# Optimization experiments

Measured on AMD Instinct MI355X. Metric: run time of the kernel, lower is better.

Reference implementation:

```python
import jax, jax.numpy as jnp
import numpy as np

D_MODEL = 512
N_HEADS = 8
D_FF = 2048
B, L = 4, 2048
EPS = 1e-5


def _layernorm(x, g, b):
    mu = jnp.mean(x, axis=-1, keepdims=True)
    var = jnp.mean(jnp.square(x - mu), axis=-1, keepdims=True)
    return (x - mu) * jax.lax.rsqrt(var + EPS) * g + b


def setup_inputs() -> dict:
    key = jax.random.key(0)
    ks = jax.random.split(key, 8)
    s = 0.02
    return {
        'x': jax.random.normal(ks[0], (B, L, D_MODEL), jnp.float32),
        'Wq': jax.random.normal(ks[1], (D_MODEL, D_MODEL), jnp.float32) * s,
        'bq': jnp.zeros((D_MODEL,), jnp.float32),
        'Wk': jax.random.normal(ks[2], (D_MODEL, D_MODEL), jnp.float32) * s,
        'bk': jnp.zeros((D_MODEL,), jnp.float32),
        'Wv': jax.random.normal(ks[3], (D_MODEL, D_MODEL), jnp.float32) * s,
        'bv': jnp.zeros((D_MODEL,), jnp.float32),
        'Wo': jax.random.normal(ks[4], (D_MODEL, D_MODEL), jnp.float32) * s,
        'bo': jnp.zeros((D_MODEL,), jnp.float32),
        'W1': jax.random.normal(ks[5], (D_MODEL, D_FF), jnp.float32) * s,
        'b1': jnp.zeros((D_FF,), jnp.float32),
        'W2': jax.random.normal(ks[6], (D_FF, D_MODEL), jnp.float32) * s,
        'b2': jnp.zeros((D_MODEL,), jnp.float32),
        'g1': jnp.ones((D_MODEL,), jnp.float32),
        'be1': jnp.zeros((D_MODEL,), jnp.float32),
        'g2': jnp.ones((D_MODEL,), jnp.float32),
        'be2': jnp.zeros((D_MODEL,), jnp.float32),
    }


def reference(x, Wq, bq, Wk, bk, Wv, bv, Wo, bo, W1, b1, W2, b2, g1, be1, g2, be2):
    B_, L_, D = x.shape
    H = N_HEADS
    E = D // H
    q = (x @ Wq + bq).reshape(B_, L_, H, E)
    k = (x @ Wk + bk).reshape(B_, L_, H, E)
    v = (x @ Wv + bv).reshape(B_, L_, H, E)
    scale = 1.0 / jnp.sqrt(jnp.float32(E))
    # full [B,H,L,S] scores (mask_flag=False -> no causal mask)
    scores = jnp.einsum('blhe,bshe->bhls', q, k)
    A = jax.nn.softmax(scale * scores, axis=-1)
    V = jnp.einsum('bhls,bshd->blhd', A, v).reshape(B_, L_, D)
    attn_out = V @ Wo + bo
    x = _layernorm(x + attn_out, g1, be1)
    h = jax.nn.gelu(x @ W1 + b1, approximate=False)  # torch nn.GELU default = exact erf
    x = _layernorm(x + (h @ W2 + b2), g2, be2)
    return x
```

## Files before the change

kernel.cpp:

```cpp
#include <hip/hip_runtime.h>
#include <math.h>

#define DM 512
#define LSEQ 2048
#define BATCH 4
#define NH 8
#define EH 64
#define DFF 2048
#define MTOK (BATCH*LSEQ)
#define QKVW 1536
#define QSCL 0.18033688011112042f

using short8  = __attribute__((ext_vector_type(8))) short;
using floatx4 = __attribute__((ext_vector_type(4))) float;

__device__ __forceinline__ short f2b(float f) {
    unsigned u = __float_as_uint(f);
    return (short)((u + 0x7FFFu + ((u >> 16) & 1u)) >> 16);
}
__device__ __forceinline__ float b2f(short s) {
    return __uint_as_float(((unsigned)(unsigned short)s) << 16);
}
__device__ __forceinline__ unsigned pack2bf(float lo, float hi) {
    return __builtin_amdgcn_perm(__float_as_uint(hi) + 0x8000u,
                                 __float_as_uint(lo) + 0x8000u, 0x07060302u);
}
__device__ __forceinline__ float gelu_tanh(float v) {
    float v2 = v * v;
    float y  = v * fmaf(0.0356774081f, v2, 0.7978845608f);
    float e  = __builtin_amdgcn_exp2f(y * 2.885390082f);
    float r  = __builtin_amdgcn_rcpf(e + 1.0f);
    return v * (1.0f - r);
}
__device__ __forceinline__ void load_lds16(const short* g, short* l) {
    __builtin_amdgcn_global_load_lds(
        (const __attribute__((address_space(1))) void*)g,
        (__attribute__((address_space(3))) void*)l, 16, 0, 0);
}
#define MFMA_BF16(a, b, c) __builtin_amdgcn_mfma_f32_16x16x32_bf16(a, b, c, 0, 0, 0)

__global__ __launch_bounds__(256) void prep_kernel(
    const float* __restrict__ Wq, const float* __restrict__ Wk,
    const float* __restrict__ Wv, const float* __restrict__ Wo,
    const float* __restrict__ W1, const float* __restrict__ W2,
    const float* __restrict__ x,
    const float* __restrict__ bq, const float* __restrict__ bk,
    const float* __restrict__ bv,
    short* __restrict__ Wqkvt, short* __restrict__ Wot,
    short* __restrict__ W1t, short* __restrict__ W2t,
    short* __restrict__ xb, float* __restrict__ bqkv)
{
    __shared__ float t[64][65];
    const int bid = blockIdx.x;
    const int tid = threadIdx.x;

    if (bid >= 2880) {
        #pragma unroll
        for (int j = 0; j < 6; ++j) {
            const int i = j * 256 + tid;
            bqkv[i] = (i < 512) ? bq[i] : (i < 1024 ? bk[i - 512] : bv[i - 1024]);
        }
        return;
    }
    if (bid >= 832) {
        const long i = ((long)(bid - 832) * 256 + tid) * 8;
        float4 a = *(const float4*)(x + i);
        float4 b = *(const float4*)(x + i + 4);
        short tt[8] = { f2b(a.x), f2b(a.y), f2b(a.z), f2b(a.w),
                        f2b(b.x), f2b(b.y), f2b(b.z), f2b(b.w) };
        *(float4*)(xb + i) = *(float4*)tt;
        return;
    }
    const float* src; short* dst; int C, R, bx, by;
    if (bid < 256) {
        const int w = bid >> 6, sub = bid & 63;
        src = (w == 0) ? Wq : (w == 1) ? Wk : Wv;
        dst = Wqkvt + (long)w * 262144;
        R = 512; C = 512; bx = sub & 7; by = sub >> 3;
    } else if (bid < 320) {
        const int sub = bid - 256;
        src = Wo; dst = Wot; R = 512; C = 512; bx = sub & 7; by = sub >> 3;
    } else if (bid < 576) {
        const int sub = bid - 320;
        src = W1; dst = W1t; R = 512; C = 2048; bx = sub & 31; by = sub >> 5;
    } else {
        const int sub = bid - 576;
        src = W2; dst = W2t; R = 2048; C = 512; bx = sub & 7; by = sub >> 3;
    }
    const int r0 = by * 64, c0 = bx * 64;
    const int r = tid >> 2, cs = (tid & 3) * 16;
    const float* ip = src + (long)(r0 + r) * C + c0 + cs;
    #pragma unroll
    for (int i = 0; i < 4; ++i) {
        float4 v = *(const float4*)(ip + i * 4);
        t[r][cs + i*4 + 0] = v.x; t[r][cs + i*4 + 1] = v.y;
        t[r][cs + i*4 + 2] = v.z; t[r][cs + i*4 + 3] = v.w;
    }
    __syncthreads();
    short tmp[16];
    #pragma unroll
    for (int j = 0; j < 16; ++j) tmp[j] = f2b(t[cs + j][r]);
    short* op = dst + (long)(c0 + r) * R + r0 + cs;
    *(float4*)op       = *(float4*)&tmp[0];
    *(float4*)(op + 8) = *(float4*)&tmp[8];
}

template<int TN, int DO_GELU, int QKV>
__global__ __launch_bounds__(256, 4) void mfma_gemm(
    const short* __restrict__ A, const short* __restrict__ Bt,
    const float* __restrict__ bias, short* __restrict__ C,
    short* __restrict__ VtOut, int M, int N, int K, int lda, int ldc)
{
    constexpr int NJ = TN / 32;
    constexpr int NB = TN / 64;
    __shared__ short As[2][128][32];
    __shared__ short Bs[2][TN][32];

    const int tid  = threadIdx.x;
    const int wave = tid >> 6;
    const int lane = tid & 63;
    const int qd   = lane >> 4;
    const int sl   = lane & 15;
    const int m0 = blockIdx.y * 128;
    const int n0 = blockIdx.x * TN;
    const int wm = (wave & 1) * 64;
    const int wn = (wave >> 1) * (TN / 2);
    const int srow = lane >> 2;
    const int scol = (lane & 3) * 8;

    floatx4 acc[4][NJ];
    const floatx4 fz = {0.f, 0.f, 0.f, 0.f};
    #pragma unroll
    for (int i = 0; i < 4; ++i)
        #pragma unroll
        for (int j = 0; j < NJ; ++j) acc[i][j] = fz;

    const short* Abase = A  + (long)m0 * lda + scol;
    const short* Bbase = Bt + (long)n0 * K   + scol;

    #pragma unroll
    for (int it = 0; it < 2; ++it) {
        const int rg = wave * 2 + it;
        load_lds16(Abase + (long)(rg*16 + srow) * lda, &As[0][rg * 16][0]);
    }
    #pragma unroll
    for (int it = 0; it < NB; ++it) {
        const int rg = wave * NB + it;
        load_lds16(Bbase + (long)(rg*16 + srow) * K, &Bs[0][rg * 16][0]);
    }

    const int NIT = K / 32;
    for (int kit = 0; kit < NIT; ++kit) {
        const int cur = kit & 1;
        __syncthreads();
        if (kit + 1 < NIT) {
            const int nk = (kit + 1) * 32;
            #pragma unroll
            for (int it = 0; it < 2; ++it) {
                const int rg = wave * 2 + it;
                load_lds16(Abase + (long)(rg*16 + srow) * lda + nk, &As[1 - cur][rg * 16][0]);
            }
            #pragma unroll
            for (int it = 0; it < NB; ++it) {
                const int rg = wave * NB + it;
                load_lds16(Bbase + (long)(rg*16 + srow) * K + nk, &Bs[1 - cur][rg * 16][0]);
            }
        }
        short8 af[4], bf[NJ];
        #pragma unroll
        for (int t = 0; t < 4; ++t)
            af[t] = *(const short8*)&As[cur][wm + t*16 + sl][qd * 8];
        #pragma unroll
        for (int t = 0; t < NJ; ++t)
            bf[t] = *(const short8*)&Bs[cur][wn + t*16 + sl][qd * 8];
        #pragma unroll
        for (int i = 0; i < 4; ++i)
            #pragma unroll
            for (int j = 0; j < NJ; ++j)
                acc[i][j] = MFMA_BF16(af[i], bf[j], acc[i][j]);
    }

    #pragma unroll
    for (int j = 0; j < NJ; ++j) {
        const int col = n0 + wn + j*16 + sl;
        const float bvs = bias[col];
        #pragma unroll
        for (int i = 0; i < 4; ++i) {
            float v[4];
            #pragma unroll
            for (int r = 0; r < 4; ++r) {
                float tv = acc[i][j][r] + bvs;
                if (DO_GELU) tv = gelu_tanh(tv);
                v[r] = tv;
            }
            const int row0 = m0 + wm + i*16 + qd*4;
            if (QKV) {
                if (col < 1024) {
                    const float s = (col < 512) ? QSCL : 1.0f;
                    #pragma unroll
                    for (int r = 0; r < 4; ++r)
                        C[(long)(row0 + r) * 1024 + col] = f2b(v[r] * s);
                } else {
                    const int e = col - 1024;
                    const int b_ = row0 >> 11, l0 = row0 & 2047;
                    uint2 w;
                    w.x = pack2bf(v[0], v[1]);
                    w.y = pack2bf(v[2], v[3]);
                    *(uint2*)&VtOut[(((long)(b_*8 + (e >> 6))) * 64 + (e & 63)) * 2048 + l0] = w;
                }
            } else {
                #pragma unroll
                for (int r = 0; r < 4; ++r)
                    C[(long)(row0 + r) * ldc + col] = f2b(v[r]);
            }
        }
    }
}

__global__ __launch_bounds__(256, 3) void mfma_attn(
    const short* __restrict__ QK, const short* __restrict__ VtG,
    short* __restrict__ O)
{
    __shared__ short Ks[2][2][64][32];
    __shared__ short Vs[2][2][64][32];
    __shared__ short PT[4][16][72];

    const int tid  = threadIdx.x;
    const int wave = tid >> 6;
    const int lane = tid & 63;
    const int qd   = lane >> 4;
    const int sl   = lane & 15;
    const int srow = lane >> 2;
    const int scol = (lane & 3) * 8;

    const int bid = blockIdx.x;
    const int h  = bid & 7;
    const int b  = (bid >> 3) & 3;
    const int qt = bid >> 5;
    const int tok0 = b * LSEQ;
    const int q0 = qt * 64;

    const short* Kbase = QK + (long)tok0 * 1024 + 512 + h * EH
                         + (long)(wave*16 + srow) * 1024 + scol;
    const short* Vbase = VtG + ((long)(b * NH + h)) * EH * 2048
                         + (long)(wave*16 + srow) * 2048 + scol;

    {
        const int qr = lane >> 2;
        const int qc = (lane & 3) * 16;
        const short* qp = QK + (long)(tok0 + q0 + wave*16 + qr) * 1024 + h * EH + qc;
        short* dp = &PT[wave][qr][qc];
        *(float4*)dp       = *(const float4*)qp;
        *(float4*)(dp + 8) = *(const float4*)(qp + 8);
    }
    short8 aq[2];
    #pragma unroll
    for (int ks = 0; ks < 2; ++ks)
        aq[ks] = *(const short8*)&PT[wave][sl][ks*32 + qd*8];

    float l_i = 0.f;
    floatx4 oacc[4];
    const floatx4 fz = {0.f, 0.f, 0.f, 0.f};
    #pragma unroll
    for (int t = 0; t < 4; ++t) oacc[t] = fz;

    #pragma unroll
    for (int p = 0; p < 2; ++p) {
        load_lds16(Kbase + p*32, &Ks[0][p][wave*16][0]);
        load_lds16(Vbase + p*32, &Vs[0][p][wave*16][0]);
    }

    for (int kt = 0; kt < 32; ++kt) {
        const int cur = kt & 1;
        __syncthreads();
        if (kt + 1 < 32) {
            #pragma unroll
            for (int p = 0; p < 2; ++p) {
                load_lds16(Kbase + (long)(kt+1)*64*1024 + p*32, &Ks[1 - cur][p][wave*16][0]);
                load_lds16(Vbase + (kt+1)*64 + p*32,            &Vs[1 - cur][p][wave*16][0]);
            }
        }

        floatx4 sT[4];
        #pragma unroll
        for (int t = 0; t < 4; ++t) sT[t] = fz;
        #pragma unroll
        for (int ks = 0; ks < 2; ++ks)
            #pragma unroll
            for (int t = 0; t < 4; ++t) {
                short8 ak = *(const short8*)&Ks[cur][ks][t*16 + sl][qd * 8];
                sT[t] = MFMA_BF16(ak, aq[ks], sT[t]);
            }

        #pragma unroll
        for (int t = 0; t < 4; ++t) {
            const float p0 = __builtin_amdgcn_exp2f(sT[t][0]);
            const float p1 = __builtin_amdgcn_exp2f(sT[t][1]);
            const float p2 = __builtin_amdgcn_exp2f(sT[t][2]);
            const float p3 = __builtin_amdgcn_exp2f(sT[t][3]);
            l_i += (p0 + p1) + (p2 + p3);
            uint2 w;
            w.x = pack2bf(p0, p1);
            w.y = pack2bf(p2, p3);
            *(uint2*)&PT[wave][sl][t*16 + qd*4] = w;
        }

        #pragma unroll
        for (int ks = 0; ks < 2; ++ks) {
            short8 ap = *(const short8*)&PT[wave][sl][ks*32 + qd*8];
            #pragma unroll
            for (int t = 0; t < 4; ++t) {
                short8 bv = *(const short8*)&Vs[cur][ks][t*16 + sl][qd * 8];
                oacc[t] = MFMA_BF16(ap, bv, oacc[t]);
            }
        }
    }

    l_i += __shfl_xor(l_i, 16);
    l_i += __shfl_xor(l_i, 32);
    float linv[4];
    #pragma unroll
    for (int r = 0; r < 4; ++r)
        linv[r] = 1.0f / __shfl(l_i, qd*4 + r, 64);

    #pragma unroll
    for (int t = 0; t < 4; ++t)
        #pragma unroll
        for (int r = 0; r < 4; ++r) {
            const int row = tok0 + q0 + wave*16 + qd*4 + r;
            const int col = h * EH + t*16 + sl;
            O[(long)row * DM + col] = f2b(oacc[t][r] * linv[r]);
        }
}

template<int X_BF16, int OUT_F32>
__global__ __launch_bounds__(256) void add_ln_kernel(
    const void* __restrict__ Xv, const short* __restrict__ R,
    const float* __restrict__ g, const float* __restrict__ beta,
    void* __restrict__ outv)
{
    const int row = blockIdx.x;
    const int tid = threadIdx.x;
    float x0, x1;
    if (X_BF16) {
        const short* xp = (const short*)Xv + (long)row * DM;
        x0 = b2f(xp[tid]); x1 = b2f(xp[tid + 256]);
    } else {
        const float* xp = (const float*)Xv + (long)row * DM;
        x0 = xp[tid]; x1 = xp[tid + 256];
    }
    const short* rp = R + (long)row * DM;
    const float v0 = x0 + b2f(rp[tid]);
    const float v1 = x1 + b2f(rp[tid + 256]);
    float s = v0 + v1, sq = v0*v0 + v1*v1;
    #pragma unroll
    for (int o = 32; o > 0; o >>= 1) {
        s  += __shfl_down(s, o);
        sq += __shfl_down(sq, o);
    }
    __shared__ float ss[4], ssq[4];
    const int wid = tid >> 6, lane = tid & 63;
    if (lane == 0) { ss[wid] = s; ssq[wid] = sq; }
    __syncthreads();
    const float S  = ss[0] + ss[1] + ss[2] + ss[3];
    const float SQ = ssq[0] + ssq[1] + ssq[2] + ssq[3];
    const float mean = S * (1.0f / DM);
    const float var  = SQ * (1.0f / DM) - mean * mean;
    const float rstd = rsqrtf(var + 1e-5f);
    const float o0 = (v0 - mean) * rstd * g[tid] + beta[tid];
    const float o1 = (v1 - mean) * rstd * g[tid + 256] + beta[tid + 256];
    if (OUT_F32) {
        float* op = (float*)outv + (long)row * DM;
        op[tid] = o0; op[tid + 256] = o1;
    } else {
        short* op = (short*)outv + (long)row * DM;
        op[tid] = f2b(o0); op[tid + 256] = f2b(o1);
    }
}

extern "C" void kernel_launch(void* const* d_in, const int* in_sizes, int n_in,
                              void* d_out, int out_size, void* d_ws, size_t ws_size,
                              hipStream_t stream)
{
    const float* x   = (const float*)d_in[0];
    const float* Wq  = (const float*)d_in[1];
    const float* bq  = (const float*)d_in[2];
    const float* Wk  = (const float*)d_in[3];
    const float* bk  = (const float*)d_in[4];
    const float* Wv  = (const float*)d_in[5];
    const float* bv  = (const float*)d_in[6];
    const float* Wo  = (const float*)d_in[7];
    const float* bo  = (const float*)d_in[8];
    const float* W1  = (const float*)d_in[9];
    const float* b1  = (const float*)d_in[10];
    const float* W2  = (const float*)d_in[11];
    const float* b2  = (const float*)d_in[12];
    const float* g1  = (const float*)d_in[13];
    const float* be1 = (const float*)d_in[14];
    const float* g2  = (const float*)d_in[15];
    const float* be2 = (const float*)d_in[16];
    float* out = (float*)d_out;

    short* ws    = (short*)d_ws;
    short* Wqkvt = ws;
    short* Wot   = Wqkvt + 786432;
    short* W1t   = Wot + 262144;
    short* W2t   = W1t + 1048576;
    float* bqkv  = (float*)(W2t + 1048576);
    short* xb    = (short*)(bqkv + 1536);
    short* qk    = xb + 4194304;
    short* VtG   = qk + 8388608;
    short* Ob    = VtG + 4194304;
    short* res   = Ob + 4194304;
    short* hbuf  = qk;

    const dim3 blk(256);

    prep_kernel<<<dim3(2881), blk, 0, stream>>>(
        Wq, Wk, Wv, Wo, W1, W2, x, bq, bk, bv,
        Wqkvt, Wot, W1t, W2t, xb, bqkv);

    mfma_gemm<128, 0, 1><<<dim3(12, 64), blk, 0, stream>>>(
        xb, Wqkvt, bqkv, qk, VtG, MTOK, QKVW, DM, DM, 0);

    mfma_attn<<<dim3(1024), blk, 0, stream>>>(qk, VtG, Ob);

    mfma_gemm<64, 0, 0><<<dim3(8, 64), blk, 0, stream>>>(
        Ob, Wot, bo, res, nullptr, MTOK, DM, DM, DM, DM);

    add_ln_kernel<0, 0><<<dim3(MTOK), blk, 0, stream>>>(x, res, g1, be1, xb);

    mfma_gemm<128, 1, 0><<<dim3(16, 64), blk, 0, stream>>>(
        xb, W1t, b1, hbuf, nullptr, MTOK, DFF, DM, DM, DFF);

    mfma_gemm<64, 0, 0><<<dim3(8, 64), blk, 0, stream>>>(
        hbuf, W2t, b2, res, nullptr, MTOK, DM, DFF, DFF, DM);

    add_ln_kernel<1, 1><<<dim3(MTOK), blk, 0, stream>>>(xb, res, g2, be2, out);
}
```

Measured before the change: 291.3 us.

## Process 32 query rows per wave in attention to reuse K/V tiles

Each wave in the attention kernel now handles two 16-row query sub-tiles instead of one, doubling the block's query tile to 128 rows and halving the grid to 512 blocks. Each K and V fragment read from LDS feeds two MFMAs, which halves K/V global and LDS traffic per query. The cost is more registers per thread (accumulators and scores are doubled), so the occupancy hint drops from 3 to 2 blocks per CU, and there are fewer blocks to spread across the CUs.

New measurement: 276.7 us. 1.05x faster.

```diff
diff --git a/kernel.cpp b/kernel.cpp
--- a/kernel.cpp
+++ b/kernel.cpp
@@ -217,13 +217,13 @@
     }
 }
 
-__global__ __launch_bounds__(256, 3) void mfma_attn(
+__global__ __launch_bounds__(256, 2) void mfma_attn(
     const short* __restrict__ QK, const short* __restrict__ VtG,
     short* __restrict__ O)
 {
     __shared__ short Ks[2][2][64][32];
     __shared__ short Vs[2][2][64][32];
-    __shared__ short PT[4][16][72];
+    __shared__ short PT[4][32][72];
 
     const int tid  = threadIdx.x;
     const int wave = tid >> 6;
@@ -238,7 +238,7 @@
     const int b  = (bid >> 3) & 3;
     const int qt = bid >> 5;
     const int tok0 = b * LSEQ;
-    const int q0 = qt * 64;
+    const int q0 = qt * 128;
 
     const short* Kbase = QK + (long)tok0 * 1024 + 512 + h * EH
                          + (long)(wave*16 + srow) * 1024 + scol;
@@ -246,23 +246,29 @@
                          + (long)(wave*16 + srow) * 2048 + scol;
 
     {
-        const int qr = lane >> 2;
-        const int qc = (lane & 3) * 16;
-        const short* qp = QK + (long)(tok0 + q0 + wave*16 + qr) * 1024 + h * EH + qc;
+        const int qr = lane >> 1;
+        const int qc = (lane & 1) * 32;
+        const short* qp = QK + (long)(tok0 + q0 + wave*32 + qr) * 1024 + h * EH + qc;
         short* dp = &PT[wave][qr][qc];
-        *(float4*)dp       = *(const float4*)qp;
-        *(float4*)(dp + 8) = *(const float4*)(qp + 8);
-    }
-    short8 aq[2];
-    #pragma unroll
-    for (int ks = 0; ks < 2; ++ks)
-        aq[ks] = *(const short8*)&PT[wave][sl][ks*32 + qd*8];
-
-    float l_i = 0.f;
-    floatx4 oacc[4];
+        *(float4*)dp        = *(const float4*)qp;
+        *(float4*)(dp + 8)  = *(const float4*)(qp + 8);
+        *(float4*)(dp + 16) = *(const float4*)(qp + 16);
+        *(float4*)(dp + 24) = *(const float4*)(qp + 24);
+    }
+    short8 aq[2][2];
+    #pragma unroll
+    for (int q2 = 0; q2 < 2; ++q2)
+        #pragma unroll
+        for (int ks = 0; ks < 2; ++ks)
+            aq[q2][ks] = *(const short8*)&PT[wave][q2*16 + sl][ks*32 + qd*8];
+
+    float l_i[2] = {0.f, 0.f};
+    floatx4 oacc[2][4];
     const floatx4 fz = {0.f, 0.f, 0.f, 0.f};
     #pragma unroll
-    for (int t = 0; t < 4; ++t) oacc[t] = fz;
+    for (int q2 = 0; q2 < 2; ++q2)
+        #pragma unroll
+        for (int t = 0; t < 4; ++t) oacc[q2][t] = fz;
 
     #pragma unroll
     for (int p = 0; p < 2; ++p) {
@@ -281,56 +287,69 @@
             }
         }
 
-        floatx4 sT[4];
-        #pragma unroll
-        for (int t = 0; t < 4; ++t) sT[t] = fz;
+        floatx4 sT[2][4];
+        #pragma unroll
+        for (int q2 = 0; q2 < 2; ++q2)
+            #pragma unroll
+            for (int t = 0; t < 4; ++t) sT[q2][t] = fz;
         #pragma unroll
         for (int ks = 0; ks < 2; ++ks)
             #pragma unroll
             for (int t = 0; t < 4; ++t) {
                 short8 ak = *(const short8*)&Ks[cur][ks][t*16 + sl][qd * 8];
-                sT[t] = MFMA_BF16(ak, aq[ks], sT[t]);
-            }
-
-        #pragma unroll
-        for (int t = 0; t < 4; ++t) {
-            const float p0 = __builtin_amdgcn_exp2f(sT[t][0]);
-            const float p1 = __builtin_amdgcn_exp2f(sT[t][1]);
-            const float p2 = __builtin_amdgcn_exp2f(sT[t][2]);
-            const float p3 = __builtin_amdgcn_exp2f(sT[t][3]);
-            l_i += (p0 + p1) + (p2 + p3);
-            uint2 w;
-            w.x = pack2bf(p0, p1);
-            w.y = pack2bf(p2, p3);
-            *(uint2*)&PT[wave][sl][t*16 + qd*4] = w;
-        }
+                sT[0][t] = MFMA_BF16(ak, aq[0][ks], sT[0][t]);
+                sT[1][t] = MFMA_BF16(ak, aq[1][ks], sT[1][t]);
+            }
+
+        #pragma unroll
+        for (int q2 = 0; q2 < 2; ++q2)
+            #pragma unroll
+            for (int t = 0; t < 4; ++t) {
+                const float p0 = __builtin_amdgcn_exp2f(sT[q2][t][0]);
+                const float p1 = __builtin_amdgcn_exp2f(sT[q2][t][1]);
+                const float p2 = __builtin_amdgcn_exp2f(sT[q2][t][2]);
+                const float p3 = __builtin_amdgcn_exp2f(sT[q2][t][3]);
+                l_i[q2] += (p0 + p1) + (p2 + p3);
+                uint2 w;
+                w.x = pack2bf(p0, p1);
+                w.y = pack2bf(p2, p3);
+                *(uint2*)&PT[wave][q2*16 + sl][t*16 + qd*4] = w;
+            }
 
         #pragma unroll
         for (int ks = 0; ks < 2; ++ks) {
-            short8 ap = *(const short8*)&PT[wave][sl][ks*32 + qd*8];
+            short8 ap0 = *(const short8*)&PT[wave][sl][ks*32 + qd*8];
+            short8 ap1 = *(const short8*)&PT[wave][16 + sl][ks*32 + qd*8];
             #pragma unroll
             for (int t = 0; t < 4; ++t) {
                 short8 bv = *(const short8*)&Vs[cur][ks][t*16 + sl][qd * 8];
-                oacc[t] = MFMA_BF16(ap, bv, oacc[t]);
+                oacc[0][t] = MFMA_BF16(ap0, bv, oacc[0][t]);
+                oacc[1][t] = MFMA_BF16(ap1, bv, oacc[1][t]);
             }
         }
     }
 
-    l_i += __shfl_xor(l_i, 16);
-    l_i += __shfl_xor(l_i, 32);
-    float linv[4];
-    #pragma unroll
-    for (int r = 0; r < 4; ++r)
-        linv[r] = 1.0f / __shfl(l_i, qd*4 + r, 64);
-
-    #pragma unroll
-    for (int t = 0; t < 4; ++t)
-        #pragma unroll
-        for (int r = 0; r < 4; ++r) {
-            const int row = tok0 + q0 + wave*16 + qd*4 + r;
-            const int col = h * EH + t*16 + sl;
-            O[(long)row * DM + col] = f2b(oacc[t][r] * linv[r]);
-        }
+    float linv[2][4];
+    #pragma unroll
+    for (int q2 = 0; q2 < 2; ++q2) {
+        float l = l_i[q2];
+        l += __shfl_xor(l, 16);
+        l += __shfl_xor(l, 32);
+        #pragma unroll
+        for (int r = 0; r < 4; ++r)
+            linv[q2][r] = 1.0f / __shfl(l, qd*4 + r, 64);
+    }
+
+    #pragma unroll
+    for (int q2 = 0; q2 < 2; ++q2)
+        #pragma unroll
+        for (int t = 0; t < 4; ++t)
+            #pragma unroll
+            for (int r = 0; r < 4; ++r) {
+                const int row = tok0 + q0 + wave*32 + q2*16 + qd*4 + r;
+                const int col = h * EH + t*16 + sl;
+                O[(long)row * DM + col] = f2b(oacc[q2][t][r] * linv[q2][r]);
+            }
 }
 
 template<int X_BF16, int OUT_F32>
@@ -423,7 +442,7 @@
     mfma_gemm<128, 0, 1><<<dim3(12, 64), blk, 0, stream>>>(
         xb, Wqkvt, bqkv, qk, VtG, MTOK, QKVW, DM, DM, 0);
 
-    mfma_attn<<<dim3(1024), blk, 0, stream>>>(qk, VtG, Ob);
+    mfma_attn<<<dim3(512), blk, 0, stream>>>(qk, VtG, Ob);
 
     mfma_gemm<64, 0, 0><<<dim3(8, 64), blk, 0, stream>>>(
         Ob, Wot, bo, res, nullptr, MTOK, DM, DM, DM, DM);
```

## Parameterize GEMM K-tile depth and double attention block to 128 queries

Applied to the files above, without the earlier changes.

The GEMM kernel gains a KB template parameter so the K-step per LDS stage can be 64 instead of 32. That halves the number of barrier-separated iterations for the QKV, Wo and W2 GEMMs, at the cost of twice the LDS and a lower occupancy bound. The attention kernel now uses 512-thread blocks covering 128 queries. Four waves load K tiles and four load V tiles, so each K/V tile staged in LDS is shared by twice as many query rows, and the grid is halved. The attention hunk is only partly visible, so whether the added waves also compute on their own query rows cannot be fully confirmed.

After: 282.5 us. 3.0% less time.

```diff
diff --git a/kernel.cpp b/kernel.cpp
--- a/kernel.cpp
+++ b/kernel.cpp
@@ -105,16 +105,19 @@
     *(float4*)(op + 8) = *(float4*)&tmp[8];
 }
 
-template<int TN, int DO_GELU, int QKV>
-__global__ __launch_bounds__(256, 4) void mfma_gemm(
+template<int TN, int KB, int DO_GELU, int QKV>
+__global__ __launch_bounds__(256, (KB == 32 ? 4 : 2)) void mfma_gemm(
     const short* __restrict__ A, const short* __restrict__ Bt,
     const float* __restrict__ bias, short* __restrict__ C,
     short* __restrict__ VtOut, int M, int N, int K, int lda, int ldc)
 {
-    constexpr int NJ = TN / 32;
-    constexpr int NB = TN / 64;
-    __shared__ short As[2][128][32];
-    __shared__ short Bs[2][TN][32];
+    constexpr int NJ  = TN / 32;
+    constexpr int KS  = KB / 32;
+    constexpr int RPI = 1024 / (KB * 2);
+    constexpr int AI  = 128 / RPI / 4;
+    constexpr int BI  = TN / RPI / 4;
+    __shared__ short As[2][128][KB];
+    __shared__ short Bs[2][TN][KB];
 
     const int tid  = threadIdx.x;
     const int wave = tid >> 6;
@@ -125,8 +128,8 @@
     const int n0 = blockIdx.x * TN;
     const int wm = (wave & 1) * 64;
     const int wn = (wave >> 1) * (TN / 2);
-    const int srow = lane >> 2;
-    const int scol = (lane & 3) * 8;
+    const int lr = lane / (KB / 8);
+    const int lc = (lane % (KB / 8)) * 8;
 
     floatx4 acc[4][NJ];
     const floatx4 fz = {0.f, 0.f, 0.f, 0.f};
@@ -135,49 +138,52 @@
         #pragma unroll
         for (int j = 0; j < NJ; ++j) acc[i][j] = fz;
 
-    const short* Abase = A  + (long)m0 * lda + scol;
-    const short* Bbase = Bt + (long)n0 * K   + scol;
-
-    #pragma unroll
-    for (int it = 0; it < 2; ++it) {
-        const int rg = wave * 2 + it;
-        load_lds16(Abase + (long)(rg*16 + srow) * lda, &As[0][rg * 16][0]);
-    }
-    #pragma unroll
-    for (int it = 0; it < NB; ++it) {
-        const int rg = wave * NB + it;
-        load_lds16(Bbase + (long)(rg*16 + srow) * K, &Bs[0][rg * 16][0]);
-    }
-
-    const int NIT = K / 32;
+    const short* Abase = A  + (long)m0 * lda + lc;
+    const short* Bbase = Bt + (long)n0 * K   + lc;
+
+    #pragma unroll
+    for (int it = 0; it < AI; ++it) {
+        const int row0 = (wave * AI + it) * RPI;
+        load_lds16(Abase + (long)(row0 + lr) * lda, &As[0][row0][0]);
+    }
+    #pragma unroll
+    for (int it = 0; it < BI; ++it) {
+        const int row0 = (wave * BI + it) * RPI;
+        load_lds16(Bbase + (long)(row0 + lr) * K, &Bs[0][row0][0]);
+    }
+
+    const int NIT = K / KB;
     for (int kit = 0; kit < NIT; ++kit) {
         const int cur = kit & 1;
         __syncthreads();
         if (kit + 1 < NIT) {
-            const int nk = (kit + 1) * 32;
-            #pragma unroll
-            for (int it = 0; it < 2; ++it) {
-                const int rg = wave * 2 + it;
-                load_lds16(Abase + (long)(rg*16 + srow) * lda + nk, &As[1 - cur][rg * 16][0]);
-            }
-            #pragma unroll
-            for (int it = 0; it < NB; ++it) {
-                const int rg = wave * NB + it;
-                load_lds16(Bbase + (long)(rg*16 + srow) * K + nk, &Bs[1 - cur][rg * 16][0]);
-            }
-        }
-        short8 af[4], bf[NJ];
-        #pragma unroll
-        for (int t = 0; t < 4; ++t)
-            af[t] = *(const short8*)&As[cur][wm + t*16 + sl][qd * 8];
-        #pragma unroll
-        for (int t = 0; t < NJ; ++t)
-            bf[t] = *(const short8*)&Bs[cur][wn + t*16 + sl][qd * 8];
-        #pragma unroll
-        for (int i = 0; i < 4; ++i)
-            #pragma unroll
-            for (int j = 0; j < NJ; ++j)
-                acc[i][j] = MFMA_BF16(af[i], bf[j], acc[i][j]);
+            const int nk = (kit + 1) * KB;
+            #pragma unroll
+            for (int it = 0; it < AI; ++it) {
+                const int row0 = (wave * AI + it) * RPI;
+                load_lds16(Abase + (long)(row0 + lr) * lda + nk, &As[1 - cur][row0][0]);
+            }
+            #pragma unroll
+            for (int it = 0; it < BI; ++it) {
+                const int row0 = (wave * BI + it) * RPI;
+                load_lds16(Bbase + (long)(row0 + lr) * K + nk, &Bs[1 - cur][row0][0]);
+            }
+        }
+        #pragma unroll
+        for (int s = 0; s < KS; ++s) {
+            short8 af[4], bf[NJ];
+            #pragma unroll
+            for (int t = 0; t < 4; ++t)
+                af[t] = *(const short8*)&As[cur][wm + t*16 + sl][s*32 + qd*8];
+            #pragma unroll
+            for (int t = 0; t < NJ; ++t)
+                bf[t] = *(const short8*)&Bs[cur][wn + t*16 + sl][s*32 + qd*8];
+            #pragma unroll
+            for (int i = 0; i < 4; ++i)
+                #pragma unroll
+                for (int j = 0; j < NJ; ++j)
+                    acc[i][j] = MFMA_BF16(af[i], bf[j], acc[i][j]);
+        }
     }
 
     #pragma unroll
@@ -217,33 +223,35 @@
     }
 }
 
-__global__ __launch_bounds__(256, 3) void mfma_attn(
+__global__ __launch_bounds__(512, 4) void mfma_attn(
     const short* __restrict__ QK, const short* __restrict__ VtG,
     short* __restrict__ O)
 {
     __shared__ short Ks[2][2][64][32];
     __shared__ short Vs[2][2][64][32];
-    __shared__ short PT[4][16][72];
+    __shared__ short PT[8][16][68];
 
     const int tid  = threadIdx.x;
     const int wave = tid >> 6;
     const int lane = tid & 63;
     const int qd   = lane >> 4;
     const int sl   = lane & 15;
+    const int kw   = wave & 3;
     const int srow = lane >> 2;
     const int scol = (lane & 3) * 8;
+    const bool is_v = wave >= 4;
 
     const int bid = blockIdx.x;
     const int h  = bid & 7;
     const int b  = (bid >> 3) & 3;
     const int qt = bid >> 5;
     const int tok0 = b * LSEQ;
-    const int q0 = qt * 64;
+    const int q0 = qt * 128;
 
     const short* Kbase = QK + (long)tok0 * 1024 + 512 + h * EH
-                         + (long)(wave*16 + srow) * 1024 + scol;
+                         + (long)(kw*16 + srow) * 1024 + scol;
     const short* Vbase = VtG + ((long)(b * NH + h)) * EH * 2048
-                         + (long)(wave*16 + srow) * 2048 + scol;
+                         + (long)(kw*16 + srow) * 2048 + scol;
 
     {
         const int qr = lane >> 2;
@@ -264,20 +272,26 @@
     #pragma unroll
     for (int t = 0; t < 4; ++t) oacc[t] = fz;
 
-    #pragma unroll
-    for (int p = 0; p < 2; ++p) {
-        load_lds16(Kbase + p*32, &Ks[0][p][wave*16][0]);
-        load_lds16(Vbase + p*32, &Vs[0][p][wave*16][0]);
+    if (!is_v) {
+        #pragma unroll
+        for (int p = 0; p < 2; ++p) load_lds16(Kbase + p*32, &Ks[0][p][kw*16][0]);
+    } else {
+        #pragma unroll
+        for (int p = 0; p < 2; ++p) load_lds16(Vbase + p*32, &Vs[0][p][kw*16][0]);
     }
 
     for (int kt = 0; kt < 32; ++kt) {
         const int cur = kt & 1;
         __syncthreads();
         if (kt + 1 < 32) {
-            #pragma unroll
-            for (int p = 0; p < 2; ++p) {
-                load_lds16(Kbase + (long)(kt+1)*64*1024 + p*32, &Ks[1 - cur][p][wave*16][0]);
-                load_lds16(Vbase + (kt+1)*64 + p*32,            &Vs[1 - cur][p][wave*16][0]);
+            if (!is_v) {
+                #pragma unroll
+                for (int p = 0; p < 2; ++p)
+                    load_lds16(Kbase + (long)(kt+1)*64*1024 + p*32, &Ks[1 - cur][p][kw*16][0]);
+            } else {
+                #pragma unroll
+                for (int p = 0; p < 2; ++p)
+                    load_lds16(Vbase + (kt+1)*64 + p*32, &Vs[1 - cur][p][kw*16][0]);
             }
         }
 
@@ -420,20 +434,20 @@
         Wq, Wk, Wv, Wo, W1, W2, x, bq, bk, bv,
         Wqkvt, Wot, W1t, W2t, xb, bqkv);
 
-    mfma_gemm<128, 0, 1><<<dim3(12, 64), blk, 0, stream>>>(
+    mfma_gemm<128, 64, 0, 1><<<dim3(12, 64), blk, 0, stream>>>(
         xb, Wqkvt, bqkv, qk, VtG, MTOK, QKVW, DM, DM, 0);
 
-    mfma_attn<<<dim3(1024), blk, 0, stream>>>(qk, VtG, Ob);
-
-    mfma_gemm<64, 0, 0><<<dim3(8, 64), blk, 0, stream>>>(
+    mfma_attn<<<dim3(512), dim3(512), 0, stream>>>(qk, VtG, Ob);
+
+    mfma_gemm<64, 64, 0, 0><<<dim3(8, 64), blk, 0, stream>>>(
         Ob, Wot, bo, res, nullptr, MTOK, DM, DM, DM, DM);
 
     add_ln_kernel<0, 0><<<dim3(MTOK), blk, 0, stream>>>(x, res, g1, be1, xb);
 
-    mfma_gemm<128, 1, 0><<<dim3(16, 64), blk, 0, stream>>>(
+    mfma_gemm<128, 32, 1, 0><<<dim3(16, 64), blk, 0, stream>>>(
         xb, W1t, b1, hbuf, nullptr, MTOK, DFF, DM, DM, DFF);
 
-    mfma_gemm<64, 0, 0><<<dim3(8, 64), blk, 0, stream>>>(
+    mfma_gemm<64, 64, 0, 0><<<dim3(8, 64), blk, 0, stream>>>(
         hbuf, W2t, b2, res, nullptr, MTOK, DM, DFF, DFF, DM);
 
     add_ln_kernel<1, 1><<<dim3(MTOK), blk, 0, stream>>>(xb, res, g2, be2, out);
```
